# Kernel tuning notes

Hardware: AMD Instinct MI355X
Metric: run time of the kernel (lower is better)

The kernel has to match this reference:

```python
import jax, jax.numpy as jnp
import numpy as np

H = 16       # num_heads
D = 128      # head_dim
SCALE = 1.0 / np.sqrt(D).astype(np.float32)


def setup_inputs() -> dict:
    key = jax.random.key(0)
    ks = jax.random.split(key, 5)
    B, S, C = 2, 2048, 2048
    x = jax.random.normal(ks[0], (B, S, C), dtype=jnp.float32)
    # nn.Linear stores weight as [out_features, in_features]; scale ~ kaiming-ish
    s = 1.0 / np.sqrt(C)
    wq = jax.random.normal(ks[1], (C, C), dtype=jnp.float32) * s
    wk = jax.random.normal(ks[2], (C, C), dtype=jnp.float32) * s
    wv = jax.random.normal(ks[3], (C, C), dtype=jnp.float32) * s
    wo = jax.random.normal(ks[4], (C, C), dtype=jnp.float32) * s
    return {"x": x, "wq": wq, "wk": wk, "wv": wv, "wo": wo}


def reference(x, wq, wk, wv, wo):
    B, S, C = x.shape
    # projections: nn.Linear(x) = x @ W.T
    q = (x @ wq.T).reshape(B, S, H, D).transpose(0, 2, 1, 3)  # [B,H,S,D]
    k = (x @ wk.T).reshape(B, S, H, D).transpose(0, 2, 1, 3)
    v = (x @ wv.T).reshape(B, S, H, D).transpose(0, 2, 1, 3)
    scores = jnp.einsum('bhqd,bhkd->bhqk', q, k) * SCALE      # [B,H,S,S]
    attn = jax.nn.softmax(scores, axis=-1)
    out = jnp.einsum('bhqk,bhkd->bhqd', attn, v)              # [B,H,S,D]
    out = out.transpose(0, 2, 1, 3).reshape(B, S, H * D)
    return out @ wo.T
```

## Files before the change

### kernel.cpp

```cpp
#include <hip/hip_runtime.h>
#include <hip/hip_bf16.h>
#include <cstdint>
#include <cstddef>

typedef __bf16 bf16_t;
typedef __bf16 bf8_t __attribute__((ext_vector_type(8)));
typedef float f4_t __attribute__((ext_vector_type(4)));
typedef float f8_t __attribute__((ext_vector_type(8)));

#define DEV static __device__ __forceinline__

DEV f4_t mfma16(bf8_t a, bf8_t b, f4_t c) {
    return __builtin_amdgcn_mfma_f32_16x16x32_bf16(a, b, c, 0, 0, 0);
}

DEV bf8_t cvt8(f8_t v) {
    bf8_t r;
#pragma unroll
    for (int i = 0; i < 8; ++i) r[i] = (bf16_t)v[i];
    return r;
}

DEV void load_lds16(const bf16_t* g, bf16_t* l) {
    __builtin_amdgcn_global_load_lds(
        (const __attribute__((address_space(1))) uint32_t*)g,
        (__attribute__((address_space(3))) uint32_t*)l,
        16, 0, 0);
}

__global__ __launch_bounds__(256) void cvt_fused(const float* __restrict__ x,
                                                 const float* __restrict__ wq,
                                                 const float* __restrict__ wk,
                                                 const float* __restrict__ wv,
                                                 bf16_t* __restrict__ xb,
                                                 bf16_t* __restrict__ wqkvb) {
    const int bid = blockIdx.x;
    const float* src;
    bf16_t* dst;
    int base;
    if (bid < 4096) {
        src = x; dst = xb; base = bid;
    } else {
        const int seg = (bid - 4096) >> 11;
        src = (seg == 0) ? wq : (seg == 1) ? wk : wv;
        dst = wqkvb + (size_t)seg * 4194304;
        base = (bid - 4096) & 2047;
    }
    const size_t i = ((size_t)base * 256 + threadIdx.x) * 8;
    const f8_t v = *(const f8_t*)&src[i];
    *(bf8_t*)&dst[i] = cvt8(v);
}

__global__ __launch_bounds__(256) void cvt_bf16(const float* __restrict__ in,
                                                bf16_t* __restrict__ out, int n8) {
    const int i = blockIdx.x * 256 + threadIdx.x;
    if (i < n8) {
        const f8_t v = *(const f8_t*)&in[(size_t)i * 8];
        *(bf8_t*)&out[(size_t)i * 8] = cvt8(v);
    }
}

template <int MODE>
__global__ __launch_bounds__(256) void gemm_m97(const bf16_t* __restrict__ A,
                                                const bf16_t* __restrict__ B,
                                                void* __restrict__ C0,
                                                bf16_t* __restrict__ C1,
                                                bf16_t* __restrict__ C2,
                                                int N, int K) {
    constexpr int SMEMN = (MODE == 0) ? 128 * 136 : 8192;
    __shared__ bf16_t smem[SMEMN];
    bf16_t* As = smem;
    bf16_t* Bs = smem + 4096;

    const int tid = threadIdx.x;
    const int lane = tid & 63;
    const int wave = tid >> 6;
    const int bm0 = blockIdx.y * 128;
    const int bn0 = blockIdx.x * 128;
    const int wm = (wave >> 1) * 64;
    const int wn = (wave & 1) * 64;
    const int q4 = lane >> 4;
    const int r16 = lane & 15;

    const int srow = lane >> 2;
    const int scol = (lane & 3) * 8;

    f4_t acc[4][4] = {};

    for (int k0 = 0; k0 < K; k0 += 32) {
        __syncthreads();
        load_lds16(A + (size_t)(bm0 + wave * 16 + srow) * K + k0 + scol, As + wave * 16 * 32);
        load_lds16(A + (size_t)(bm0 + 64 + wave * 16 + srow) * K + k0 + scol,
                   As + (64 + wave * 16) * 32);
        load_lds16(B + (size_t)(bn0 + wave * 16 + srow) * K + k0 + scol, Bs + wave * 16 * 32);
        load_lds16(B + (size_t)(bn0 + 64 + wave * 16 + srow) * K + k0 + scol,
                   Bs + (64 + wave * 16) * 32);
        __syncthreads();

        bf8_t af[4], bfr[4];
#pragma unroll
        for (int i = 0; i < 4; ++i)
            af[i] = *(const bf8_t*)&As[(wm + i * 16 + r16) * 32 + q4 * 8];
#pragma unroll
        for (int j = 0; j < 4; ++j)
            bfr[j] = *(const bf8_t*)&Bs[(wn + j * 16 + r16) * 32 + q4 * 8];
#pragma unroll
        for (int i = 0; i < 4; ++i)
#pragma unroll
            for (int j = 0; j < 4; ++j)
                acc[i][j] = mfma16(af[i], bfr[j], acc[i][j]);
    }

    if (MODE == 1) {
        float* C = (float*)C0;
#pragma unroll
        for (int i = 0; i < 4; ++i)
#pragma unroll
            for (int j = 0; j < 4; ++j)
#pragma unroll
                for (int r = 0; r < 4; ++r) {
                    const int m = bm0 + wm + i * 16 + q4 * 4 + r;
                    const int n = bn0 + wn + j * 16 + r16;
                    C[(size_t)m * 2048 + n] = acc[i][j][r];
                }
        return;
    }

    if (bn0 < 4096) {
        bf16_t* dst = (bn0 < 2048) ? (bf16_t*)C0 : C1;
        const int nbase = bn0 & 2047;
#pragma unroll
        for (int i = 0; i < 4; ++i)
#pragma unroll
            for (int j = 0; j < 4; ++j)
#pragma unroll
                for (int r = 0; r < 4; ++r) {
                    const int m = bm0 + wm + i * 16 + q4 * 4 + r;
                    const int n = nbase + wn + j * 16 + r16;
                    dst[(size_t)m * 2048 + n] = (bf16_t)acc[i][j][r];
                }
    } else {
        __syncthreads();
#pragma unroll
        for (int i = 0; i < 4; ++i)
#pragma unroll
            for (int j = 0; j < 4; ++j)
#pragma unroll
                for (int r = 0; r < 4; ++r)
                    smem[(wn + j * 16 + r16) * 136 + wm + i * 16 + q4 * 4 + r] =
                        (bf16_t)acc[i][j][r];
        __syncthreads();
        const int bb = bm0 >> 11;
        const int s0 = bm0 & 2047;
        const int nh0 = bn0 - 4096;
#pragma unroll
        for (int it = 0; it < 8; ++it) {
            const int idx = it * 256 + tid;
            const int n = idx >> 4;
            const int mc = (idx & 15) * 8;
            const bf8_t v = *(const bf8_t*)&smem[n * 136 + mc];
            const int dg = nh0 + n;
            const int h = dg >> 7, d = dg & 127;
            *(bf8_t*)&C2[(((size_t)(bb * 16 + h) * 128 + d) << 11) + s0 + mc] = v;
        }
    }
}

__global__ __launch_bounds__(512) void flash4(const bf16_t* __restrict__ Q,
                                              const bf16_t* __restrict__ K,
                                              const bf16_t* __restrict__ VT,
                                              bf16_t* __restrict__ O) {
    constexpr int S = 2048, C = 2048;
    constexpr float SCL = 0.08838834764831845f * 1.4426950408889634f;
    __shared__ bf16_t Ks[4 * 64 * 32];
    __shared__ bf16_t Vs[2 * 128 * 32];
    __shared__ bf16_t Ps[8][16 * 72];

    const int tid = threadIdx.x, lane = tid & 63, wave = tid >> 6;
    const int q4 = lane >> 4, r16 = lane & 15;
    const int bh = blockIdx.y, b = bh >> 4, h = bh & 15;
    const int q0 = blockIdx.x * 128 + wave * 16;

    const size_t qrow = (size_t)b * S + q0;
    const bf16_t* Qp = Q + (qrow + r16) * C + h * 128;
    const bf16_t* Kbase = K + (size_t)b * S * C + h * 128;
    const bf16_t* Vbase = VT + (size_t)bh * 128 * S;
    bf16_t* Pw = &Ps[wave][0];

    const int srow = lane >> 2;
    const int scol = (lane & 3) * 8;

    bf8_t aq[4];
#pragma unroll
    for (int kk = 0; kk < 4; ++kk) aq[kk] = *(const bf8_t*)&Qp[kk * 32 + q4 * 8];

    bf8_t ones;
#pragma unroll
    for (int i = 0; i < 8; ++i) ones[i] = (bf16_t)1.0f;

    f4_t o[8] = {};
    f4_t lacc = {};

    const int id0 = wave * 2, id1 = wave * 2 + 1;

    for (int kv0 = 0; kv0 < S; kv0 += 64) {
        __syncthreads();
        {
            const int dc0 = id0 >> 2, rs0 = id0 & 3;
            load_lds16(Kbase + (size_t)(kv0 + rs0 * 16 + srow) * C + dc0 * 32 + scol,
                       Ks + dc0 * 2048 + rs0 * 512);
            const int dc1 = id1 >> 2, rs1 = id1 & 3;
            load_lds16(Kbase + (size_t)(kv0 + rs1 * 16 + srow) * C + dc1 * 32 + scol,
                       Ks + dc1 * 2048 + rs1 * 512);
        }
        {
            const int kc0 = id0 >> 3, rs0 = id0 & 7;
            load_lds16(Vbase + (size_t)(rs0 * 16 + srow) * S + kv0 + kc0 * 32 + scol,
                       Vs + kc0 * 4096 + rs0 * 512);
            const int kc1 = id1 >> 3, rs1 = id1 & 7;
            load_lds16(Vbase + (size_t)(rs1 * 16 + srow) * S + kv0 + kc1 * 32 + scol,
                       Vs + kc1 * 4096 + rs1 * 512);
        }
        __syncthreads();

        f4_t s4[4] = {};
#pragma unroll
        for (int kk = 0; kk < 4; ++kk) {
#pragma unroll
            for (int j = 0; j < 4; ++j) {
                const bf8_t bk = *(const bf8_t*)&Ks[kk * 2048 + (j * 16 + r16) * 32 + q4 * 8];
                s4[j] = mfma16(aq[kk], bk, s4[j]);
            }
        }

#pragma unroll
        for (int r = 0; r < 4; ++r)
#pragma unroll
            for (int j = 0; j < 4; ++j)
                Pw[(q4 * 4 + r) * 72 + j * 16 + r16] = (bf16_t)exp2f(s4[j][r] * SCL);
        asm volatile("s_waitcnt lgkmcnt(0)" ::: "memory");

        bf8_t ap[2];
#pragma unroll
        for (int kkp = 0; kkp < 2; ++kkp)
            ap[kkp] = *(const bf8_t*)&Pw[r16 * 72 + kkp * 32 + q4 * 8];

#pragma unroll
        for (int kkp = 0; kkp < 2; ++kkp) lacc = mfma16(ap[kkp], ones, lacc);

#pragma unroll
        for (int t = 0; t < 8; ++t) {
#pragma unroll
            for (int kkp = 0; kkp < 2; ++kkp) {
                const bf8_t bv =
                    *(const bf8_t*)&Vs[kkp * 4096 + (t * 16 + r16) * 32 + q4 * 8];
                o[t] = mfma16(ap[kkp], bv, o[t]);
            }
        }
    }

    f4_t inv;
#pragma unroll
    for (int r = 0; r < 4; ++r) inv[r] = 1.0f / lacc[r];
#pragma unroll
    for (int t = 0; t < 8; ++t)
#pragma unroll
        for (int r = 0; r < 4; ++r)
            O[(qrow + q4 * 4 + r) * C + h * 128 + t * 16 + r16] = (bf16_t)(o[t][r] * inv[r]);
}

extern "C" void kernel_launch(void* const* d_in, const int* in_sizes, int n_in,
                              void* d_out, int out_size, void* d_ws, size_t ws_size,
                              hipStream_t stream) {
    const float* x  = (const float*)d_in[0];
    const float* wq = (const float*)d_in[1];
    const float* wk = (const float*)d_in[2];
    const float* wv = (const float*)d_in[3];
    const float* wo = (const float*)d_in[4];

    bf16_t* ws = (bf16_t*)d_ws;
    bf16_t* xb   = ws;
    bf16_t* Wqkv = ws + 8388608;
    bf16_t* Qb   = ws + 20971520;
    bf16_t* Kb   = ws + 29360128;
    bf16_t* Vt   = ws + 37748736;
    bf16_t* Wob  = xb;
    bf16_t* At   = Wqkv;

    cvt_fused<<<10240, 256, 0, stream>>>(x, wq, wk, wv, xb, Wqkv);

    gemm_m97<0><<<dim3(48, 32), 256, 0, stream>>>(xb, Wqkv, Qb, Kb, Vt, 6144, 2048);

    cvt_bf16<<<2048, 256, 0, stream>>>(wo, Wob, 524288);

    flash4<<<dim3(16, 32), 512, 0, stream>>>(Qb, Kb, Vt, At);

    gemm_m97<1><<<dim3(16, 32), 256, 0, stream>>>(At, Wob, d_out, nullptr, nullptr, 2048, 2048);
}
```

Before: 430.3 us.

## Swizzle LDS tiles, stage GEMM stores through LDS, give flash waves 32 query rows

Applies an XOR swizzle to the LDS column index for the GEMM and flash K/V tiles so that MFMA fragment reads avoid LDS bank conflicts. In the QKV GEMM, the Q and K outputs are staged through shared memory and written as coalesced 16-byte rows instead of scattered 2-byte stores. The flash kernel drops to 256 threads, and each wave now processes 32 query rows instead of 16, reusing each K/V fragment read across two MFMA chains. This doubles accumulator register use per wave and halves the number of waves per block, which may lower occupancy.

After: 426.8 us. No clear change (-0.8%).

```diff
diff --git a/kernel.cpp b/kernel.cpp
--- a/kernel.cpp
+++ b/kernel.cpp
@@ -83,7 +83,8 @@
     const int r16 = lane & 15;
 
     const int srow = lane >> 2;
-    const int scol = (lane & 3) * 8;
+    const int scol = (((lane & 3) ^ ((lane >> 3) & 3))) * 8;
+    const int rkey = (r16 >> 1) & 3;
 
     f4_t acc[4][4] = {};
 
@@ -100,10 +101,10 @@
         bf8_t af[4], bfr[4];
 #pragma unroll
         for (int i = 0; i < 4; ++i)
-            af[i] = *(const bf8_t*)&As[(wm + i * 16 + r16) * 32 + q4 * 8];
+            af[i] = *(const bf8_t*)&As[(wm + i * 16 + r16) * 32 + (q4 ^ rkey) * 8];
 #pragma unroll
         for (int j = 0; j < 4; ++j)
-            bfr[j] = *(const bf8_t*)&Bs[(wn + j * 16 + r16) * 32 + q4 * 8];
+            bfr[j] = *(const bf8_t*)&Bs[(wn + j * 16 + r16) * 32 + (q4 ^ rkey) * 8];
 #pragma unroll
         for (int i = 0; i < 4; ++i)
 #pragma unroll
@@ -126,6 +127,7 @@
         return;
     }
 
+    __syncthreads();
     if (bn0 < 4096) {
         bf16_t* dst = (bn0 < 2048) ? (bf16_t*)C0 : C1;
         const int nbase = bn0 & 2047;
@@ -134,13 +136,19 @@
 #pragma unroll
             for (int j = 0; j < 4; ++j)
 #pragma unroll
-                for (int r = 0; r < 4; ++r) {
-                    const int m = bm0 + wm + i * 16 + q4 * 4 + r;
-                    const int n = nbase + wn + j * 16 + r16;
-                    dst[(size_t)m * 2048 + n] = (bf16_t)acc[i][j][r];
-                }
+                for (int r = 0; r < 4; ++r)
+                    smem[(wm + i * 16 + q4 * 4 + r) * 136 + wn + j * 16 + r16] =
+                        (bf16_t)acc[i][j][r];
+        __syncthreads();
+#pragma unroll
+        for (int it = 0; it < 8; ++it) {
+            const int idx = it * 256 + tid;
+            const int m = idx >> 4;
+            const int nc = (idx & 15) * 8;
+            *(bf8_t*)&dst[(size_t)(bm0 + m) * 2048 + nbase + nc] =
+                *(const bf8_t*)&smem[m * 136 + nc];
+        }
     } else {
-        __syncthreads();
 #pragma unroll
         for (int i = 0; i < 4; ++i)
 #pragma unroll
@@ -166,7 +174,7 @@
     }
 }
 
-__global__ __launch_bounds__(512) void flash4(const bf16_t* __restrict__ Q,
+__global__ __launch_bounds__(256) void flash5(const bf16_t* __restrict__ Q,
                                               const bf16_t* __restrict__ K,
                                               const bf16_t* __restrict__ VT,
                                               bf16_t* __restrict__ O) {
@@ -174,99 +182,114 @@
     constexpr float SCL = 0.08838834764831845f * 1.4426950408889634f;
     __shared__ bf16_t Ks[4 * 64 * 32];
     __shared__ bf16_t Vs[2 * 128 * 32];
-    __shared__ bf16_t Ps[8][16 * 72];
+    __shared__ bf16_t Ps[4][32 * 72];
 
     const int tid = threadIdx.x, lane = tid & 63, wave = tid >> 6;
     const int q4 = lane >> 4, r16 = lane & 15;
     const int bh = blockIdx.y, b = bh >> 4, h = bh & 15;
-    const int q0 = blockIdx.x * 128 + wave * 16;
+    const int q0 = blockIdx.x * 128 + wave * 32;
 
     const size_t qrow = (size_t)b * S + q0;
-    const bf16_t* Qp = Q + (qrow + r16) * C + h * 128;
+    const bf16_t* Qp0 = Q + (qrow + r16) * C + h * 128;
+    const bf16_t* Qp1 = Q + (qrow + 16 + r16) * C + h * 128;
     const bf16_t* Kbase = K + (size_t)b * S * C + h * 128;
     const bf16_t* Vbase = VT + (size_t)bh * 128 * S;
     bf16_t* Pw = &Ps[wave][0];
 
     const int srow = lane >> 2;
-    const int scol = (lane & 3) * 8;
-
-    bf8_t aq[4];
-#pragma unroll
-    for (int kk = 0; kk < 4; ++kk) aq[kk] = *(const bf8_t*)&Qp[kk * 32 + q4 * 8];
+    const int scol = (((lane & 3) ^ ((lane >> 3) & 3))) * 8;
+    const int rkey = (r16 >> 1) & 3;
+
+    bf8_t aq0[4], aq1[4];
+#pragma unroll
+    for (int kk = 0; kk < 4; ++kk) {
+        aq0[kk] = *(const bf8_t*)&Qp0[kk * 32 + q4 * 8];
+        aq1[kk] = *(const bf8_t*)&Qp1[kk * 32 + q4 * 8];
+    }
 
     bf8_t ones;
 #pragma unroll
     for (int i = 0; i < 8; ++i) ones[i] = (bf16_t)1.0f;
 
-    f4_t o[8] = {};
-    f4_t lacc = {};
-
-    const int id0 = wave * 2, id1 = wave * 2 + 1;
+    f4_t o0[8] = {}, o1[8] = {};
+    f4_t lacc0 = {}, lacc1 = {};
 
     for (int kv0 = 0; kv0 < S; kv0 += 64) {
         __syncthreads();
+#pragma unroll
+        for (int r0 = 0; r0 < 64; r0 += 16)
+            load_lds16(Kbase + (size_t)(kv0 + r0 + srow) * C + wave * 32 + scol,
+                       Ks + wave * 2048 + r0 * 32);
         {
-            const int dc0 = id0 >> 2, rs0 = id0 & 3;
-            load_lds16(Kbase + (size_t)(kv0 + rs0 * 16 + srow) * C + dc0 * 32 + scol,
-                       Ks + dc0 * 2048 + rs0 * 512);
-            const int dc1 = id1 >> 2, rs1 = id1 & 3;
-            load_lds16(Kbase + (size_t)(kv0 + rs1 * 16 + srow) * C + dc1 * 32 + scol,
-                       Ks + dc1 * 2048 + rs1 * 512);
-        }
-        {
-            const int kc0 = id0 >> 3, rs0 = id0 & 7;
-            load_lds16(Vbase + (size_t)(rs0 * 16 + srow) * S + kv0 + kc0 * 32 + scol,
-                       Vs + kc0 * 4096 + rs0 * 512);
-            const int kc1 = id1 >> 3, rs1 = id1 & 7;
-            load_lds16(Vbase + (size_t)(rs1 * 16 + srow) * S + kv0 + kc1 * 32 + scol,
-                       Vs + kc1 * 4096 + rs1 * 512);
-        }
-        __syncthreads();
-
-        f4_t s4[4] = {};
+            const int kkp = wave >> 1;
+            const int rb = (wave & 1) * 64;
+#pragma unroll
+            for (int r0 = 0; r0 < 64; r0 += 16)
+                load_lds16(Vbase + (size_t)(rb + r0 + srow) * S + kv0 + kkp * 32 + scol,
+                           Vs + kkp * 4096 + (rb + r0) * 32);
+        }
+        __syncthreads();
+
+        f4_t s4a[4] = {}, s4b[4] = {};
 #pragma unroll
         for (int kk = 0; kk < 4; ++kk) {
 #pragma unroll
             for (int j = 0; j < 4; ++j) {
-                const bf8_t bk = *(const bf8_t*)&Ks[kk * 2048 + (j * 16 + r16) * 32 + q4 * 8];
-                s4[j] = mfma16(aq[kk], bk, s4[j]);
+                const bf8_t bk =
+                    *(const bf8_t*)&Ks[kk * 2048 + (j * 16 + r16) * 32 + (q4 ^ rkey) * 8];
+                s4a[j] = mfma16(aq0[kk], bk, s4a[j]);
+                s4b[j] = mfma16(aq1[kk], bk, s4b[j]);
             }
         }
 
 #pragma unroll
         for (int r = 0; r < 4; ++r)
 #pragma unroll
-            for (int j = 0; j < 4; ++j)
-                Pw[(q4 * 4 + r) * 72 + j * 16 + r16] = (bf16_t)exp2f(s4[j][r] * SCL);
+            for (int j = 0; j < 4; ++j) {
+                Pw[(q4 * 4 + r) * 72 + j * 16 + r16] = (bf16_t)exp2f(s4a[j][r] * SCL);
+                Pw[(16 + q4 * 4 + r) * 72 + j * 16 + r16] = (bf16_t)exp2f(s4b[j][r] * SCL);
+            }
         asm volatile("s_waitcnt lgkmcnt(0)" ::: "memory");
 
-        bf8_t ap[2];
-#pragma unroll
-        for (int kkp = 0; kkp < 2; ++kkp)
-            ap[kkp] = *(const bf8_t*)&Pw[r16 * 72 + kkp * 32 + q4 * 8];
-
-#pragma unroll
-        for (int kkp = 0; kkp < 2; ++kkp) lacc = mfma16(ap[kkp], ones, lacc);
+        bf8_t ap0[2], ap1[2];
+#pragma unroll
+        for (int kkp = 0; kkp < 2; ++kkp) {
+            ap0[kkp] = *(const bf8_t*)&Pw[r16 * 72 + kkp * 32 + q4 * 8];
+            ap1[kkp] = *(const bf8_t*)&Pw[(16 + r16) * 72 + kkp * 32 + q4 * 8];
+        }
+
+#pragma unroll
+        for (int kkp = 0; kkp < 2; ++kkp) {
+            lacc0 = mfma16(ap0[kkp], ones, lacc0);
+            lacc1 = mfma16(ap1[kkp], ones, lacc1);
+        }
 
 #pragma unroll
         for (int t = 0; t < 8; ++t) {
 #pragma unroll
             for (int kkp = 0; kkp < 2; ++kkp) {
                 const bf8_t bv =
-                    *(const bf8_t*)&Vs[kkp * 4096 + (t * 16 + r16) * 32 + q4 * 8];
-                o[t] = mfma16(ap[kkp], bv, o[t]);
+                    *(const bf8_t*)&Vs[kkp * 4096 + (t * 16 + r16) * 32 + (q4 ^ rkey) * 8];
+                o0[t] = mfma16(ap0[kkp], bv, o0[t]);
+                o1[t] = mfma16(ap1[kkp], bv, o1[t]);
             }
         }
     }
 
-    f4_t inv;
-#pragma unroll
-    for (int r = 0; r < 4; ++r) inv[r] = 1.0f / lacc[r];
+    f4_t inv0, inv1;
+#pragma unroll
+    for (int r = 0; r < 4; ++r) {
+        inv0[r] = 1.0f / lacc0[r];
+        inv1[r] = 1.0f / lacc1[r];
+    }
 #pragma unroll
     for (int t = 0; t < 8; ++t)
 #pragma unroll
-        for (int r = 0; r < 4; ++r)
-            O[(qrow + q4 * 4 + r) * C + h * 128 + t * 16 + r16] = (bf16_t)(o[t][r] * inv[r]);
+        for (int r = 0; r < 4; ++r) {
+            O[(qrow + q4 * 4 + r) * C + h * 128 + t * 16 + r16] = (bf16_t)(o0[t][r] * inv0[r]);
+            O[(qrow + 16 + q4 * 4 + r) * C + h * 128 + t * 16 + r16] =
+                (bf16_t)(o1[t][r] * inv1[r]);
+        }
 }
 
 extern "C" void kernel_launch(void* const* d_in, const int* in_sizes, int n_in,
@@ -293,7 +316,7 @@
 
     cvt_bf16<<<2048, 256, 0, stream>>>(wo, Wob, 524288);
 
-    flash4<<<dim3(16, 32), 512, 0, stream>>>(Qb, Kb, Vt, At);
+    flash5<<<dim3(16, 32), 256, 0, stream>>>(Qb, Kb, Vt, At);
 
     gemm_m97<1><<<dim3(16, 32), 256, 0, stream>>>(At, Wob, d_out, nullptr, nullptr, 2048, 2048);
 }
```
